# Kernel tuning notes

Measured on AMD Instinct MI355X. Metric: run time of the kernel, lower is better.

## Reference

```python
import jax, jax.numpy as jnp
import numpy as np

EPS = 1e-5
B, M, N, D = 8, 4096, 1024, 1024


def setup_inputs() -> dict:
    key = jax.random.key(0)
    kx, kw, kb, kg, kbe = jax.random.split(key, 5)
    return {
        "x": jax.random.normal(kx, (B, M, N), dtype=jnp.float32),
        "w": jax.random.normal(kw, (N, D), dtype=jnp.float32) * 0.02,
        "b": jax.random.normal(kb, (D,), dtype=jnp.float32) * 0.02,
        "gamma": jax.random.uniform(kg, (N,), dtype=jnp.float32, minval=0.5, maxval=1.5),
        "beta": jax.random.normal(kbe, (N,), dtype=jnp.float32) * 0.02,
    }


def reference(x, w, b, gamma, beta):
    # Fused LayerNorm (over last dim, biased variance, eps=1e-5) + matmul + bias.
    mean = jnp.mean(x, axis=-1, keepdims=True)                 # [B,M,1]
    var = jnp.mean(jnp.square(x - mean), axis=-1, keepdims=True)
    rstd = jax.lax.rsqrt(var + EPS)                            # [B,M,1]
    ln = (x - mean) * rstd * gamma + beta                      # [B,M,N]
    return jnp.einsum('bmn,nd->bmd', ln, w) + b                # [B,M,D]
```

## Files before the change

kernel.cpp:

```cpp
#include <hip/hip_runtime.h>
#include <stdint.h>

#define RROWS 32768
#define KDIM  1024
#define DDIM  1024

typedef __bf16 bf16;
typedef __bf16 bf16x4 __attribute__((ext_vector_type(4)));
typedef __bf16 bf16x8 __attribute__((ext_vector_type(8)));
typedef float  f32x4  __attribute__((ext_vector_type(4)));

typedef __attribute__((address_space(1))) const unsigned int* gas_ptr;
typedef __attribute__((address_space(3))) unsigned int* las_ptr;

__global__ __launch_bounds__(256) void prep_gt(const float* __restrict__ w,
                                               const float* __restrict__ gamma,
                                               bf16* __restrict__ Gt) {
    __shared__ float tile[64][65];
    const int k0 = blockIdx.x * 64;
    const int d0 = blockIdx.y * 64;
    const int t  = threadIdx.x;
    const int col4 = (t & 15) * 4;
    const int rowb = t >> 4;
#pragma unroll
    for (int r = 0; r < 4; ++r) {
        const int k = rowb + r * 16;
        const float4 v = *(const float4*)&w[(size_t)(k0 + k) * DDIM + d0 + col4];
        const float g = gamma[k0 + k];
        tile[k][col4 + 0] = v.x * g;
        tile[k][col4 + 1] = v.y * g;
        tile[k][col4 + 2] = v.z * g;
        tile[k][col4 + 3] = v.w * g;
    }
    __syncthreads();
#pragma unroll
    for (int r = 0; r < 2; ++r) {
        const int d  = (t >> 3) + r * 32;
        const int ks = (t & 7) * 8;
        bf16x8 o;
#pragma unroll
        for (int j = 0; j < 8; ++j) o[j] = (bf16)tile[ks + j][d];
        *(bf16x8*)&Gt[(size_t)(d0 + d) * KDIM + k0 + ks] = o;
    }
}

__global__ __launch_bounds__(256) void prep_part(const float* __restrict__ w,
                                                 const float* __restrict__ gamma,
                                                 const float* __restrict__ beta,
                                                 float* __restrict__ partG,
                                                 float* __restrict__ partB) {
    const int d  = blockIdx.x * 256 + threadIdx.x;
    const int kc = blockIdx.y;
    float ag = 0.f, ab = 0.f;
    for (int k = kc * 64; k < kc * 64 + 64; ++k) {
        const float wv = w[(size_t)k * DDIM + d];
        ag += gamma[k] * wv;
        ab += beta[k] * wv;
    }
    partG[(size_t)kc * DDIM + d] = ag;
    partB[(size_t)kc * DDIM + d] = ab;
}

__global__ __launch_bounds__(256) void prep_reduce(const float* __restrict__ partG,
                                                   const float* __restrict__ partB,
                                                   const float* __restrict__ b,
                                                   float* __restrict__ gw,
                                                   float* __restrict__ cvec) {
    const int d = blockIdx.x * 256 + threadIdx.x;
    float g = 0.f, a = 0.f;
#pragma unroll
    for (int j = 0; j < 16; ++j) {
        g += partG[(size_t)j * DDIM + d];
        a += partB[(size_t)j * DDIM + d];
    }
    gw[d]   = g;
    cvec[d] = a + b[d];
}

#define BM 128
#define BN 128
#define BK 32
#define APAD 40

__global__ __launch_bounds__(256) void fused_gemm(const float* __restrict__ x,
                                                  const bf16* __restrict__ Gt,
                                                  const float* __restrict__ gw,
                                                  const float* __restrict__ cvec,
                                                  float* __restrict__ out) {
    __shared__ __align__(16) bf16 As[BM * APAD];
    __shared__ __align__(16) bf16 Bs[BM * BK];
    __shared__ float meanS[BM];
    __shared__ float rstdS[BM];

    const int t     = threadIdx.x;
    const int mTile = blockIdx.x;
    const int dTile = blockIdx.y;
    const int row0  = mTile * BM;
    const int col0  = dTile * BN;

    const int wave = t >> 6;
    const int lane = t & 63;
    const int wr   = wave >> 1;
    const int wc   = wave & 1;

    const int a_row = t >> 3;
    const int a_seg = t & 7;

    float s1[4] = {0.f, 0.f, 0.f, 0.f};
    float s2[4] = {0.f, 0.f, 0.f, 0.f};

    f32x4 acc[4][4];
#pragma unroll
    for (int i = 0; i < 4; ++i)
#pragma unroll
        for (int j = 0; j < 4; ++j) acc[i][j] = (f32x4)0.0f;

    for (int k0 = 0; k0 < KDIM; k0 += BK) {
        __syncthreads();

#pragma unroll
        for (int j = 0; j < 2; ++j) {
            const int off  = j * 4096 + t * 16;
            const int brow = off >> 6;
            const int kseg = (off & 63) >> 1;
            const bf16* gp = Gt + (size_t)(col0 + brow) * KDIM + k0 + kseg;
            char* lp = (char*)Bs + off;
            __builtin_amdgcn_global_load_lds((gas_ptr)(const void*)gp,
                                             (las_ptr)(void*)lp, 16, 0, 0);
        }

#pragma unroll
        for (int r = 0; r < 4; ++r) {
            const int row = r * 32 + a_row;
            const float4 v = *(const float4*)&x[(size_t)(row0 + row) * KDIM + k0 + a_seg * 4];
            s1[r] += v.x + v.y + v.z + v.w;
            s2[r] += v.x * v.x + v.y * v.y + v.z * v.z + v.w * v.w;
            bf16x4 pk;
            pk[0] = (bf16)v.x; pk[1] = (bf16)v.y; pk[2] = (bf16)v.z; pk[3] = (bf16)v.w;
            *(bf16x4*)&As[row * APAD + a_seg * 4] = pk;
        }

        __syncthreads();

        bf16x8 af[4], bfr[4];
        const int arow = wr * 64 + (lane & 15);
        const int brow = wc * 64 + (lane & 15);
        const int koff = (lane >> 4) * 8;
#pragma unroll
        for (int i = 0; i < 4; ++i)
            af[i] = *(const bf16x8*)&As[(arow + i * 16) * APAD + koff];
#pragma unroll
        for (int j = 0; j < 4; ++j)
            bfr[j] = *(const bf16x8*)&Bs[(brow + j * 16) * BK + koff];
#pragma unroll
        for (int i = 0; i < 4; ++i)
#pragma unroll
            for (int j = 0; j < 4; ++j)
                acc[i][j] = __builtin_amdgcn_mfma_f32_16x16x32_bf16(af[i], bfr[j], acc[i][j], 0, 0, 0);
    }

#pragma unroll
    for (int r = 0; r < 4; ++r) {
        float a = s1[r], b = s2[r];
#pragma unroll
        for (int ofs = 1; ofs < 8; ofs <<= 1) {
            a += __shfl_xor(a, ofs, 64);
            b += __shfl_xor(b, ofs, 64);
        }
        if (a_seg == 0) {
            const int row = r * 32 + a_row;
            const float mean = a * (1.0f / KDIM);
            const float var  = b * (1.0f / KDIM) - mean * mean;
            meanS[row] = mean;
            rstdS[row] = rsqrtf(var + 1e-5f);
        }
    }
    __syncthreads();

    const int lr = (lane >> 4) * 4;
    const int lc = lane & 15;
#pragma unroll
    for (int j = 0; j < 4; ++j) {
        const int colL = wc * 64 + j * 16 + lc;
        const int col  = col0 + colL;
        const float gwv = gw[col];
        const float cv  = cvec[col];
#pragma unroll
        for (int i = 0; i < 4; ++i) {
#pragma unroll
            for (int rg = 0; rg < 4; ++rg) {
                const int rowL = wr * 64 + i * 16 + lr + rg;
                const float v = rstdS[rowL] * (acc[i][j][rg] - meanS[rowL] * gwv) + cv;
                out[(size_t)(row0 + rowL) * DDIM + col] = v;
            }
        }
    }
}

extern "C" void kernel_launch(void* const* d_in, const int* in_sizes, int n_in,
                              void* d_out, int out_size, void* d_ws, size_t ws_size,
                              hipStream_t stream) {
    const float* x     = (const float*)d_in[0];
    const float* w     = (const float*)d_in[1];
    const float* b     = (const float*)d_in[2];
    const float* gamma = (const float*)d_in[3];
    const float* beta  = (const float*)d_in[4];
    float* out = (float*)d_out;

    char* ws = (char*)d_ws;
    bf16*  Gt    = (bf16*)ws;
    float* partG = (float*)(ws + (2u << 20));
    float* partB = (float*)(ws + (2u << 20) + (64u << 10));
    float* gw    = (float*)(ws + (2u << 20) + (128u << 10));
    float* cvec  = (float*)(ws + (2u << 20) + (132u << 10));

    prep_gt<<<dim3(16, 16), 256, 0, stream>>>(w, gamma, Gt);
    prep_part<<<dim3(4, 16), 256, 0, stream>>>(w, gamma, beta, partG, partB);
    prep_reduce<<<4, 256, 0, stream>>>(partG, partB, b, gw, cvec);
    fused_gemm<<<dim3(256, 8), 256, 0, stream>>>(x, Gt, gw, cvec, out);
}
```

Measured before the change: 381.3 us.

## Split LayerNorm into a bf16 pre-pass and feed a swizzled bf16 GEMM

Adds a separate pass that normalizes each row of x and writes it as bf16 to workspace. A new GEMM then streams both operands into LDS through direct global-to-LDS loads, using BK=64 and an XOR-swizzled layout. This drops the per-tile fp32 load, convert and statistics work from the GEMM inner loop and halves A-operand traffic inside the GEMM, at the cost of an extra full read of x plus a 64MB bf16 write and re-read. When the workspace is too small, the old fused kernel is still used.

```diff
diff --git a/kernel.cpp b/kernel.cpp
--- a/kernel.cpp
+++ b/kernel.cpp
@@ -77,9 +77,141 @@
     cvec[d] = a + b[d];
 }
 
+__global__ __launch_bounds__(256) void ln_convert(const float* __restrict__ x,
+                                                  bf16* __restrict__ xb) {
+    const int wave = threadIdx.x >> 6;
+    const int lane = threadIdx.x & 63;
+    const int row  = blockIdx.x * 4 + wave;
+    const float4* xr = (const float4*)(x + (size_t)row * KDIM);
+
+    float4 v[4];
+    float s1 = 0.f, s2 = 0.f;
+#pragma unroll
+    for (int j = 0; j < 4; ++j) {
+        v[j] = xr[lane + j * 64];
+        s1 += v[j].x + v[j].y + v[j].z + v[j].w;
+        s2 += v[j].x * v[j].x + v[j].y * v[j].y + v[j].z * v[j].z + v[j].w * v[j].w;
+    }
+#pragma unroll
+    for (int ofs = 1; ofs < 64; ofs <<= 1) {
+        s1 += __shfl_xor(s1, ofs, 64);
+        s2 += __shfl_xor(s2, ofs, 64);
+    }
+    const float mean = s1 * (1.0f / KDIM);
+    const float var  = s2 * (1.0f / KDIM) - mean * mean;
+    const float rstd = rsqrtf(var + 1e-5f);
+
+    bf16x4* xo = (bf16x4*)(xb + (size_t)row * KDIM);
+#pragma unroll
+    for (int j = 0; j < 4; ++j) {
+        bf16x4 o;
+        o[0] = (bf16)((v[j].x - mean) * rstd);
+        o[1] = (bf16)((v[j].y - mean) * rstd);
+        o[2] = (bf16)((v[j].z - mean) * rstd);
+        o[3] = (bf16)((v[j].w - mean) * rstd);
+        xo[lane + j * 64] = o;
+    }
+}
+
 #define BM 128
 #define BN 128
-#define BK 32
+#define BK 64
+
+__global__ __launch_bounds__(256) void gemm_bt(const bf16* __restrict__ xb,
+                                               const bf16* __restrict__ Gt,
+                                               const float* __restrict__ cvec,
+                                               float* __restrict__ out) {
+    __shared__ __align__(16) bf16 As[BM * BK];
+    __shared__ __align__(16) bf16 Bs[BN * BK];
+
+    const int t     = threadIdx.x;
+    const int dTile = blockIdx.x;
+    const int mTile = blockIdx.y;
+    const int row0  = mTile * BM;
+    const int col0  = dTile * BN;
+
+    const int wave = t >> 6;
+    const int lane = t & 63;
+    const int wr   = wave >> 1;
+    const int wc   = wave & 1;
+    const int quad = lane >> 4;
+    const int r16  = lane & 15;
+
+    f32x4 acc[4][4];
+#pragma unroll
+    for (int i = 0; i < 4; ++i)
+#pragma unroll
+        for (int j = 0; j < 4; ++j) acc[i][j] = (f32x4)0.0f;
+
+    for (int k0 = 0; k0 < KDIM; k0 += BK) {
+        __syncthreads();
+
+#pragma unroll
+        for (int j = 0; j < 4; ++j) {
+            const int ci   = j * 256 + t;
+            const int row  = ci >> 3;
+            const int slot = ci & 7;
+            const int q    = slot ^ (row & 7);
+            const bf16* gp = xb + (size_t)(row0 + row) * KDIM + k0 + q * 8;
+            char* lp = (char*)As + ci * 16;
+            __builtin_amdgcn_global_load_lds((gas_ptr)(const void*)gp,
+                                             (las_ptr)(void*)lp, 16, 0, 0);
+        }
+#pragma unroll
+        for (int j = 0; j < 4; ++j) {
+            const int ci   = j * 256 + t;
+            const int row  = ci >> 3;
+            const int slot = ci & 7;
+            const int q    = slot ^ (row & 7);
+            const bf16* gp = Gt + (size_t)(col0 + row) * KDIM + k0 + q * 8;
+            char* lp = (char*)Bs + ci * 16;
+            __builtin_amdgcn_global_load_lds((gas_ptr)(const void*)gp,
+                                             (las_ptr)(void*)lp, 16, 0, 0);
+        }
+
+        __syncthreads();
+
+#pragma unroll
+        for (int kk = 0; kk < 2; ++kk) {
+            bf16x8 af[4], bfr[4];
+#pragma unroll
+            for (int i = 0; i < 4; ++i) {
+                const int row  = wr * 64 + i * 16 + r16;
+                const int slot = (kk * 4 + quad) ^ (row & 7);
+                af[i] = *(const bf16x8*)&As[row * BK + slot * 8];
+            }
+#pragma unroll
+            for (int j = 0; j < 4; ++j) {
+                const int row  = wc * 64 + j * 16 + r16;
+                const int slot = (kk * 4 + quad) ^ (row & 7);
+                bfr[j] = *(const bf16x8*)&Bs[row * BK + slot * 8];
+            }
+#pragma unroll
+            for (int i = 0; i < 4; ++i)
+#pragma unroll
+                for (int j = 0; j < 4; ++j)
+                    acc[i][j] = __builtin_amdgcn_mfma_f32_16x16x32_bf16(af[i], bfr[j], acc[i][j], 0, 0, 0);
+        }
+    }
+
+    const int lr = quad * 4;
+    const int lc = r16;
+#pragma unroll
+    for (int j = 0; j < 4; ++j) {
+        const int col = col0 + wc * 64 + j * 16 + lc;
+        const float cv = cvec[col];
+#pragma unroll
+        for (int i = 0; i < 4; ++i) {
+#pragma unroll
+            for (int rg = 0; rg < 4; ++rg) {
+                const int row = row0 + wr * 64 + i * 16 + lr + rg;
+                out[(size_t)row * DDIM + col] = acc[i][j][rg] + cv;
+            }
+        }
+    }
+}
+
+#define FBK 32
 #define APAD 40
 
 __global__ __launch_bounds__(256) void fused_gemm(const float* __restrict__ x,
@@ -87,8 +219,8 @@
                                                   const float* __restrict__ gw,
                                                   const float* __restrict__ cvec,
                                                   float* __restrict__ out) {
-    __shared__ __align__(16) bf16 As[BM * APAD];
-    __shared__ __align__(16) bf16 Bs[BM * BK];
+    __shared__ __align__(16) bf16 As2[BM * APAD];
+    __shared__ __align__(16) bf16 Bs2[BM * FBK];
     __shared__ float meanS[BM];
     __shared__ float rstdS[BM];
 
@@ -97,38 +229,33 @@
     const int dTile = blockIdx.y;
     const int row0  = mTile * BM;
     const int col0  = dTile * BN;
-
     const int wave = t >> 6;
     const int lane = t & 63;
     const int wr   = wave >> 1;
     const int wc   = wave & 1;
-
     const int a_row = t >> 3;
     const int a_seg = t & 7;
 
     float s1[4] = {0.f, 0.f, 0.f, 0.f};
     float s2[4] = {0.f, 0.f, 0.f, 0.f};
-
     f32x4 acc[4][4];
 #pragma unroll
     for (int i = 0; i < 4; ++i)
 #pragma unroll
         for (int j = 0; j < 4; ++j) acc[i][j] = (f32x4)0.0f;
 
-    for (int k0 = 0; k0 < KDIM; k0 += BK) {
+    for (int k0 = 0; k0 < KDIM; k0 += FBK) {
         __syncthreads();
-
 #pragma unroll
         for (int j = 0; j < 2; ++j) {
             const int off  = j * 4096 + t * 16;
             const int brow = off >> 6;
             const int kseg = (off & 63) >> 1;
             const bf16* gp = Gt + (size_t)(col0 + brow) * KDIM + k0 + kseg;
-            char* lp = (char*)Bs + off;
+            char* lp = (char*)Bs2 + off;
             __builtin_amdgcn_global_load_lds((gas_ptr)(const void*)gp,
                                              (las_ptr)(void*)lp, 16, 0, 0);
         }
-
 #pragma unroll
         for (int r = 0; r < 4; ++r) {
             const int row = r * 32 + a_row;
@@ -137,9 +264,8 @@
             s2[r] += v.x * v.x + v.y * v.y + v.z * v.z + v.w * v.w;
             bf16x4 pk;
             pk[0] = (bf16)v.x; pk[1] = (bf16)v.y; pk[2] = (bf16)v.z; pk[3] = (bf16)v.w;
-            *(bf16x4*)&As[row * APAD + a_seg * 4] = pk;
-        }
-
+            *(bf16x4*)&As2[row * APAD + a_seg * 4] = pk;
+        }
         __syncthreads();
 
         bf16x8 af[4], bfr[4];
@@ -148,10 +274,10 @@
         const int koff = (lane >> 4) * 8;
 #pragma unroll
         for (int i = 0; i < 4; ++i)
-            af[i] = *(const bf16x8*)&As[(arow + i * 16) * APAD + koff];
+            af[i] = *(const bf16x8*)&As2[(arow + i * 16) * APAD + koff];
 #pragma unroll
         for (int j = 0; j < 4; ++j)
-            bfr[j] = *(const bf16x8*)&Bs[(brow + j * 16) * BK + koff];
+            bfr[j] = *(const bf16x8*)&Bs2[(brow + j * 16) * FBK + koff];
 #pragma unroll
         for (int i = 0; i < 4; ++i)
 #pragma unroll
@@ -181,8 +307,7 @@
     const int lc = lane & 15;
 #pragma unroll
     for (int j = 0; j < 4; ++j) {
-        const int colL = wc * 64 + j * 16 + lc;
-        const int col  = col0 + colL;
+        const int col = col0 + wc * 64 + j * 16 + lc;
         const float gwv = gw[col];
         const float cv  = cvec[col];
 #pragma unroll
@@ -190,8 +315,8 @@
 #pragma unroll
             for (int rg = 0; rg < 4; ++rg) {
                 const int rowL = wr * 64 + i * 16 + lr + rg;
-                const float v = rstdS[rowL] * (acc[i][j][rg] - meanS[rowL] * gwv) + cv;
-                out[(size_t)(row0 + rowL) * DDIM + col] = v;
+                const float vv = rstdS[rowL] * (acc[i][j][rg] - meanS[rowL] * gwv) + cv;
+                out[(size_t)(row0 + rowL) * DDIM + col] = vv;
             }
         }
     }
@@ -208,14 +333,31 @@
     float* out = (float*)d_out;
 
     char* ws = (char*)d_ws;
-    bf16*  Gt    = (bf16*)ws;
-    float* partG = (float*)(ws + (2u << 20));
-    float* partB = (float*)(ws + (2u << 20) + (64u << 10));
-    float* gw    = (float*)(ws + (2u << 20) + (128u << 10));
-    float* cvec  = (float*)(ws + (2u << 20) + (132u << 10));
-
-    prep_gt<<<dim3(16, 16), 256, 0, stream>>>(w, gamma, Gt);
-    prep_part<<<dim3(4, 16), 256, 0, stream>>>(w, gamma, beta, partG, partB);
-    prep_reduce<<<4, 256, 0, stream>>>(partG, partB, b, gw, cvec);
-    fused_gemm<<<dim3(256, 8), 256, 0, stream>>>(x, Gt, gw, cvec, out);
-}
+    const size_t XB_B = (size_t)RROWS * KDIM * sizeof(bf16);
+    bf16*  xb    = (bf16*)ws;
+    bf16*  Gt    = (bf16*)(ws + XB_B);
+    float* partG = (float*)(ws + XB_B + (2u << 20));
+    float* partB = (float*)(ws + XB_B + (2u << 20) + (64u << 10));
+    float* gw    = (float*)(ws + XB_B + (2u << 20) + (128u << 10));
+    float* cvec  = (float*)(ws + XB_B + (2u << 20) + (132u << 10));
+
+    const bool big_ws = ws_size >= XB_B + (3u << 20);
+
+    if (big_ws) {
+        prep_gt<<<dim3(16, 16), 256, 0, stream>>>(w, gamma, Gt);
+        prep_part<<<dim3(4, 16), 256, 0, stream>>>(w, gamma, beta, partG, partB);
+        prep_reduce<<<4, 256, 0, stream>>>(partG, partB, b, gw, cvec);
+        ln_convert<<<RROWS / 4, 256, 0, stream>>>(x, xb);
+        gemm_bt<<<dim3(8, 256), 256, 0, stream>>>(xb, Gt, cvec, out);
+    } else {
+        bf16*  Gt2    = (bf16*)ws;
+        float* partG2 = (float*)(ws + (2u << 20));
+        float* partB2 = (float*)(ws + (2u << 20) + (64u << 10));
+        float* gw2    = (float*)(ws + (2u << 20) + (128u << 10));
+        float* cvec2  = (float*)(ws + (2u << 20) + (132u << 10));
+        prep_gt<<<dim3(16, 16), 256, 0, stream>>>(w, gamma, Gt2);
+        prep_part<<<dim3(4, 16), 256, 0, stream>>>(w, gamma, beta, partG2, partB2);
+        prep_reduce<<<4, 256, 0, stream>>>(partG2, partB2, b, gw2, cvec2);
+        fused_gemm<<<dim3(256, 8), 256, 0, stream>>>(x, Gt2, gw2, cvec2, out);
+    }
+}
```

Measured after the change: 339.1 us. -11.1%, faster.
